# Kernel optimization log

Measured on AMD Instinct MI355X. Metric: run time of the kernel, lower is better.

Reference implementation:

```python
import jax, jax.numpy as jnp
import numpy as np

B, T, NC, NK, H, W = 2, 4, 3, 16, 180, 320
K = 3
PAD = 1
SCALE = 4
K2 = K * K
CIN_D = T * NK  # deformable conv input channels = group_of_frames * num_kernels


def conv2d(x, w, b=None, pad=PAD):
    y = jax.lax.conv_general_dilated(
        x, w, (1, 1), [(pad, pad), (pad, pad)],
        dimension_numbers=('NCHW', 'OIHW', 'NCHW'))
    if b is not None:
        y = y + b[None, :, None, None]
    return y


def convlstm(X, w, b, W_ci, W_cf, W_co):
    # X: (B, T, NC, H, W) -> (B, T, NK, H, W); peephole ConvLSTM
    Bn = X.shape[0]
    h0 = jnp.zeros((Bn, NK, H, W), X.dtype)
    c0 = jnp.zeros_like(h0)

    def step(carry, xt):
        h, c = carry
        g = conv2d(jnp.concatenate([xt, h], axis=1), w, b)  # (B, 4*NK, H, W)
        ig, fg, cg, og = jnp.split(g, 4, axis=1)
        i = jax.nn.sigmoid(ig + W_ci * c)
        f = jax.nn.sigmoid(fg + W_cf * c)
        c = f * c + i * jnp.tanh(cg)
        o = jax.nn.sigmoid(og + W_co * c)
        h = o * jnp.tanh(c)
        return (h, c), h

    _, hs = jax.lax.scan(step, (h0, c0), jnp.swapaxes(X, 0, 1))
    return jnp.swapaxes(hs, 0, 1)  # (B, T, NK, H, W)


def deform_conv(x, off_w, off_b, mod_w, mod_b, w, b):
    # Modulated deformable conv v2 (torchvision deform_conv2d semantics)
    Bn, Cin, Hi, Wi = x.shape
    off = conv2d(x, off_w, off_b).reshape(Bn, K2, 2, Hi, Wi)  # (dy, dx) per tap
    mask = 2.0 * jax.nn.sigmoid(conv2d(x, mod_w, mod_b))       # (B, K2, H, W)
    dy, dx = off[:, :, 0], off[:, :, 1]
    ky, kx = jnp.meshgrid(jnp.arange(K), jnp.arange(K), indexing='ij')
    base_y = jnp.arange(Hi, dtype=x.dtype)[None, None, :, None] - PAD + ky.reshape(1, K2, 1, 1).astype(x.dtype)
    base_x = jnp.arange(Wi, dtype=x.dtype)[None, None, None, :] - PAD + kx.reshape(1, K2, 1, 1).astype(x.dtype)
    py = base_y + dy  # (B, K2, H, W) float sampling positions
    px = base_x + dx
    y0 = jnp.floor(py)
    x0 = jnp.floor(px)

    def gather(yi, xi):
        valid = ((yi >= 0) & (yi < Hi) & (xi >= 0) & (xi < Wi)).astype(x.dtype)
        yc = jnp.clip(yi, 0, Hi - 1).astype(jnp.int32)
        xc = jnp.clip(xi, 0, Wi - 1).astype(jnp.int32)
        v = jax.vmap(lambda xb, yb, xib: xb[:, yb, xib])(x, yc, xc)  # (B, C, K2, H, W)
        return v * valid[:, None]

    wy1 = py - y0
    wx1 = px - x0
    samp = (((1 - wy1) * (1 - wx1))[:, None] * gather(y0, x0)
            + ((1 - wy1) * wx1)[:, None] * gather(y0, x0 + 1)
            + (wy1 * (1 - wx1))[:, None] * gather(y0 + 1, x0)
            + (wy1 * wx1)[:, None] * gather(y0 + 1, x0 + 1))
    samp = samp * mask[:, None]  # (B, Cin, K2, H, W)
    out = jnp.einsum('bckhw,ock->bohw', samp, w.reshape(w.shape[0], Cin, K2))
    return out + b[None, :, None, None]


def pixel_shuffle(x, r):
    Bn, Crr, Hi, Wi = x.shape
    C = Crr // (r * r)
    x = x.reshape(Bn, C, r, r, Hi, Wi).transpose(0, 1, 4, 2, 5, 3)
    return x.reshape(Bn, C, Hi * r, Wi * r)


def setup_inputs() -> dict:
    key = jax.random.key(0)
    ks = jax.random.split(key, 16)
    s = lambda k, shape, sc=0.05: jax.random.normal(k, shape, jnp.float32) * sc
    return {
        'X': jax.random.uniform(ks[0], (B, T, NC, H, W), jnp.float32),
        'lstm_w': s(ks[1], (4 * NK, NC + NK, K, K)),
        'lstm_b': s(ks[2], (4 * NK,)),
        'W_ci': s(ks[3], (NK, H, W)),
        'W_cf': s(ks[4], (NK, H, W)),
        'W_co': s(ks[5], (NK, H, W)),
        'off_w': s(ks[6], (2 * K2, CIN_D, K, K), 0.01),
        'off_b': jnp.zeros((2 * K2,), jnp.float32),
        'mod_w': s(ks[7], (K2, CIN_D, K, K), 0.01),
        'mod_b': jnp.zeros((K2,), jnp.float32),
        'def_w': s(ks[8], (NK, CIN_D, K, K)),
        'def_b': s(ks[9], (NK,)),
        'out_w': s(ks[10], (NC * SCALE ** 2, NK, K, K)),
        'out_b': s(ks[11], (NC * SCALE ** 2,)),
    }


def reference(X, lstm_w, lstm_b, W_ci, W_cf, W_co, off_w, off_b, mod_w, mod_b, def_w, def_b, out_w, out_b):
    hs = convlstm(X, lstm_w, lstm_b, W_ci, W_cf, W_co)   # (B, T, NK, H, W)
    x = hs.reshape(hs.shape[0], T * NK, H, W)            # chunk(dim=1)+squeeze+cat(dim=1)
    x = deform_conv(x, off_w, off_b, mod_w, mod_b, def_w, def_b)  # (B, NK, H, W)
    x = conv2d(x, out_w, out_b)                          # (B, NC*scale^2, H, W)
    return jnp.clip(pixel_shuffle(x, SCALE), 0.0, 255.0)
```

## Files before the change

kernel.cpp:

```cpp
#include <hip/hip_runtime.h>
#include <hip/hip_bf16.h>

#define Bn 2
#define Tn 4
#define NCc 3
#define NKc 16
#define Hc 180
#define Wc 320
#define HWc (Hc * Wc)
#define NPIX (Bn * HWc)
#define CIN_LSTM 19
#define GATES 64
#define CIN_D 64
#define TAPS_L (CIN_LSTM * 9)
#define TAPS_D (CIN_D * 9)
#define TAPS_O (NKc * 9)

typedef __hip_bfloat16 bf16;
typedef float f32x4 __attribute__((ext_vector_type(4)));
typedef float f32x2 __attribute__((ext_vector_type(2)));

__device__ __forceinline__ float getv(const float* p, long i) { return p[i]; }
__device__ __forceinline__ float getv(const bf16* p, long i) {
    unsigned int u = ((unsigned int)((const unsigned short*)p)[i]) << 16;
    return __uint_as_float(u);
}
__device__ __forceinline__ void putv(float* p, long i, float v) { p[i] = v; }
__device__ __forceinline__ void putv(bf16* p, long i, float v) { p[i] = __float2bfloat16(v); }
__device__ __forceinline__ float sigm(float x) { return 1.0f / (1.0f + __expf(-x)); }
__device__ __forceinline__ float tanh_(float x) { return 1.0f - 2.0f / (__expf(2.0f * x) + 1.0f); }

__device__ __forceinline__ void load4(const float* row, int x0, float* d) {
    const float4 v = *(const float4*)(row + x0);
    d[0] = v.x; d[1] = v.y; d[2] = v.z; d[3] = v.w;
}
__device__ __forceinline__ void load4(const bf16* row, int x0, float* d) {
    ushort4 u = *(const ushort4*)((const unsigned short*)row + x0);
    d[0] = __uint_as_float(((unsigned int)u.x) << 16);
    d[1] = __uint_as_float(((unsigned int)u.y) << 16);
    d[2] = __uint_as_float(((unsigned int)u.z) << 16);
    d[3] = __uint_as_float(((unsigned int)u.w) << 16);
}

__device__ __forceinline__ int xcd_chunked(int i, int nwg) {
    int q = nwg >> 3, r = nwg & 7;
    int xcd = i & 7, idx = i >> 3;
    return (xcd < r ? xcd * (q + 1) : r * (q + 1) + (xcd - r) * q) + idx;
}

__device__ __forceinline__ void om_wait()
{
    asm volatile("s_waitcnt vmcnt(0)" ::: "memory");
    __builtin_amdgcn_sched_barrier(0);
}

__device__ __forceinline__ void om6_issue(
    const float* a0p, const float* a1p, const float* a2p,
    const float* b0p, const float* b1p, const float* b2p,
    f32x4& A0, f32x4& A1, f32x4& A2, f32x4& B0, f32x4& B1, f32x4& B2)
{
    asm volatile(
        "global_load_dwordx4 %[A0], %[a0], off\n\t"
        "global_load_dwordx4 %[A1], %[a1], off\n\t"
        "global_load_dwordx4 %[A2], %[a2], off\n\t"
        "global_load_dwordx4 %[B0], %[b0], off\n\t"
        "global_load_dwordx4 %[B1], %[b1], off\n\t"
        "global_load_dwordx4 %[B2], %[b2], off\n\t"
        : [A0]"=&v"(A0), [A1]"=&v"(A1), [A2]"=&v"(A2),
          [B0]"=&v"(B0), [B1]"=&v"(B1), [B2]"=&v"(B2)
        : [a0]"v"(a0p), [a1]"v"(a1p), [a2]"v"(a2p),
          [b0]"v"(b0p), [b1]"v"(b1p), [b2]"v"(b2p));
}

__device__ __forceinline__ void lstm_issue12(
    const float* p0, const float* p1, const float* p2, const float* p3,
    f32x4& a0, float& l0, float& r0,
    f32x4& a1, float& l1, float& r1,
    f32x4& a2, float& l2, float& r2,
    f32x4& a3, float& l3, float& r3)
{
    asm volatile(
        "global_load_dwordx4 %[A0], %[P0], off\n\t"
        "global_load_dword   %[L0], %[P0], off offset:-4\n\t"
        "global_load_dword   %[R0], %[P0], off offset:16\n\t"
        "global_load_dwordx4 %[A1], %[P1], off\n\t"
        "global_load_dword   %[L1], %[P1], off offset:-4\n\t"
        "global_load_dword   %[R1], %[P1], off offset:16\n\t"
        "global_load_dwordx4 %[A2], %[P2], off\n\t"
        "global_load_dword   %[L2], %[P2], off offset:-4\n\t"
        "global_load_dword   %[R2], %[P2], off offset:16\n\t"
        "global_load_dwordx4 %[A3], %[P3], off\n\t"
        "global_load_dword   %[L3], %[P3], off offset:-4\n\t"
        "global_load_dword   %[R3], %[P3], off offset:16\n\t"
        : [A0]"=&v"(a0), [L0]"=&v"(l0), [R0]"=&v"(r0),
          [A1]"=&v"(a1), [L1]"=&v"(l1), [R1]"=&v"(r1),
          [A2]"=&v"(a2), [L2]"=&v"(l2), [R2]"=&v"(r2),
          [A3]"=&v"(a3), [L3]"=&v"(l3), [R3]"=&v"(r3)
        : [P0]"v"(p0), [P1]"v"(p1), [P2]"v"(p2), [P3]"v"(p3));
}

__device__ __forceinline__ void dfm_issue9w(
    const float* base, const int (&o)[9], f32x2 (&v)[9])
{
    asm volatile(
        "global_load_dwordx2 %[V0], %[O0], %[B]\n\t"
        "global_load_dwordx2 %[V1], %[O1], %[B]\n\t"
        "global_load_dwordx2 %[V2], %[O2], %[B]\n\t"
        "global_load_dwordx2 %[V3], %[O3], %[B]\n\t"
        "global_load_dwordx2 %[V4], %[O4], %[B]\n\t"
        "global_load_dwordx2 %[V5], %[O5], %[B]\n\t"
        "global_load_dwordx2 %[V6], %[O6], %[B]\n\t"
        "global_load_dwordx2 %[V7], %[O7], %[B]\n\t"
        "global_load_dwordx2 %[V8], %[O8], %[B]\n\t"
        : [V0]"=&v"(v[0]), [V1]"=&v"(v[1]), [V2]"=&v"(v[2]),
          [V3]"=&v"(v[3]), [V4]"=&v"(v[4]), [V5]"=&v"(v[5]),
          [V6]"=&v"(v[6]), [V7]"=&v"(v[7]), [V8]"=&v"(v[8])
        : [B]"s"(base),
          [O0]"v"(o[0]), [O1]"v"(o[1]), [O2]"v"(o[2]),
          [O3]"v"(o[3]), [O4]"v"(o[4]), [O5]"v"(o[5]),
          [O6]"v"(o[6]), [O7]"v"(o[7]), [O8]"v"(o[8]));
}

__global__ void __launch_bounds__(256) k_detect(const void* lstm_w_raw, int* flag)
{
    __shared__ int bad;
    if (threadIdx.x == 0) bad = 0;
    __syncthreads();
    const unsigned short* u = (const unsigned short*)lstm_w_raw;
    int local = 0;
    for (int i = threadIdx.x; i < GATES * TAPS_L; i += 256) {
        unsigned int f32 = ((unsigned int)u[i]) << 16;
        float v = __uint_as_float(f32);
        if (!(fabsf(v) <= 64.0f)) local = 1;
    }
    if (local) atomicOr(&bad, 1);
    __syncthreads();
    if (threadIdx.x == 0) flag[0] = bad ? 0 : 1;
}

template <typename S>
__device__ __forceinline__ void conv_plane2r(
    const S* __restrict__ src, int cin, int y0, int x0, int kc,
    const float* __restrict__ sw, float (&acc)[2][4][4])
{
    float xs[4][6];
#pragma unroll
    for (int r = 0; r < 4; r++) {
        int yy = y0 - 1 + r;
        if (yy >= 0 && yy < Hc) {
            const S* row = src + (long)yy * Wc;
            xs[r][0] = (x0 > 0) ? getv(row, x0 - 1) : 0.0f;
            load4(row, x0, &xs[r][1]);
            xs[r][5] = (x0 + 4 < Wc) ? getv(row, x0 + 4) : 0.0f;
        } else {
#pragma unroll
            for (int j = 0; j < 6; j++) xs[r][j] = 0.0f;
        }
    }
    float4 wq[9];
#pragma unroll
    for (int t9 = 0; t9 < 9; t9++)
        wq[t9] = *(const float4*)&sw[(((cin * 9 + t9) * 16) + kc) * 4];
#pragma unroll
    for (int ky = 0; ky < 3; ky++) {
#pragma unroll
        for (int kx = 0; kx < 3; kx++) {
            const float4 w = wq[ky * 3 + kx];
#pragma unroll
            for (int px = 0; px < 4; px++) {
                float v0 = xs[ky][px + kx];
                float v1 = xs[ky + 1][px + kx];
                acc[0][0][px] += w.x * v0;  acc[1][0][px] += w.x * v1;
                acc[0][1][px] += w.y * v0;  acc[1][1][px] += w.y * v1;
                acc[0][2][px] += w.z * v0;  acc[1][2][px] += w.z * v1;
                acc[0][3][px] += w.w * v0;  acc[1][3][px] += w.w * v1;
            }
        }
    }
}

template <typename T>
__device__ __forceinline__ void lstm2r_body(
    const T* __restrict__ X, const T* __restrict__ lstm_w, const T* __restrict__ lstm_b,
    const T* __restrict__ Wci, const T* __restrict__ Wcf, const T* __restrict__ Wco,
    float* __restrict__ c_buf, float* __restrict__ xcat, int t,
    float* sw, float* sb)
{
    for (int i = threadIdx.x; i < GATES * TAPS_L; i += 256) {
        int co = i / TAPS_L, tap = i - co * TAPS_L;
        int kc = co & 15, g = co >> 4;
        sw[(tap * 16 + kc) * 4 + g] = getv(lstm_w, i);
    }
    if (threadIdx.x < GATES) sb[threadIdx.x] = getv(lstm_b, threadIdx.x);
    __syncthreads();

    int blk = xcd_chunked(blockIdx.x, Bn * 90 * 5);
    int seg = blk % 5; int rem = blk / 5;
    int yp = rem % 90; int b = rem / 90;
    int y0 = yp * 2;
    int kc = threadIdx.x >> 4, pl = threadIdx.x & 15;
    int x0 = seg * 64 + pl * 4;

    float acc[2][4][4];
#pragma unroll
    for (int px = 0; px < 4; px++) {
#pragma unroll
        for (int r = 0; r < 2; r++) {
            acc[r][0][px] = sb[kc];
            acc[r][1][px] = sb[16 + kc];
            acc[r][2][px] = sb[32 + kc];
            acc[r][3][px] = sb[48 + kc];
        }
    }

    const T* xt = X + (long)(b * Tn + t) * NCc * HWc;
#pragma unroll 1
    for (int cin = 0; cin < NCc; cin++)
        conv_plane2r(xt + (long)cin * HWc, cin, y0, x0, kc, sw, acc);

    if (t > 0) {
        const float* hp = xcat + ((long)b * CIN_D + (t - 1) * NKc) * HWc;
        long ro[4]; float vm[4];
#pragma unroll
        for (int r = 0; r < 4; r++) {
            int yy = y0 - 1 + r;
            vm[r] = (yy >= 0 && yy < Hc) ? 1.0f : 0.0f;
            ro[r] = (long)min(max(yy, 0), Hc - 1) * Wc + x0;
        }
        const float m0 = (x0 > 0) ? 1.0f : 0.0f;
        const float m1 = (x0 + 4 < Wc) ? 1.0f : 0.0f;

#pragma unroll 1
        for (int cin = 0; cin < NKc; cin++) {
            const float* xc = hp + (long)cin * HWc;
            f32x4 a0, a1, a2, a3;
            float l0, l1, l2, l3, rh0, rh1, rh2, rh3;
            lstm_issue12(xc + ro[0], xc + ro[1], xc + ro[2], xc + ro[3],
                         a0, l0, rh0, a1, l1, rh1, a2, l2, rh2, a3, l3, rh3);
            float4 wq[9];
#pragma unroll
            for (int t9 = 0; t9 < 9; t9++)
                wq[t9] = *(const float4*)&sw[((((cin + NCc) * 9 + t9) * 16) + kc) * 4];
            om_wait();
            float xs[4][6];
#pragma unroll
            for (int r = 0; r < 4; r++) {
                const f32x4 a = (r == 0) ? a0 : (r == 1) ? a1 : (r == 2) ? a2 : a3;
                const float ll = (r == 0) ? l0 : (r == 1) ? l1 : (r == 2) ? l2 : l3;
                const float rr = (r == 0) ? rh0 : (r == 1) ? rh1 : (r == 2) ? rh2 : rh3;
                xs[r][0] = ll * vm[r] * m0;
                xs[r][1] = a.x * vm[r]; xs[r][2] = a.y * vm[r];
                xs[r][3] = a.z * vm[r]; xs[r][4] = a.w * vm[r];
                xs[r][5] = rr * vm[r] * m1;
            }
#pragma unroll
            for (int ky = 0; ky < 3; ky++) {
#pragma unroll
                for (int kx = 0; kx < 3; kx++) {
                    const float4 w = wq[ky * 3 + kx];
#pragma unroll
                    for (int px = 0; px < 4; px++) {
                        float v0 = xs[ky][px + kx];
                        float v1 = xs[ky + 1][px + kx];
                        acc[0][0][px] += w.x * v0;  acc[1][0][px] += w.x * v1;
                        acc[0][1][px] += w.y * v0;  acc[1][1][px] += w.y * v1;
                        acc[0][2][px] += w.z * v0;  acc[1][2][px] += w.z * v1;
                        acc[0][3][px] += w.w * v0;  acc[1][3][px] += w.w * v1;
                    }
                }
            }
        }
    }

#pragma unroll
    for (int r = 0; r < 2; r++) {
        int y = y0 + r;
        long pbase = (long)y * Wc + x0;
        float* cb = c_buf + (long)(b * NKc + kc) * HWc + pbase;
        float cprev[4];
        if (t > 0) {
            const float4 cv = *(const float4*)cb;
            cprev[0] = cv.x; cprev[1] = cv.y; cprev[2] = cv.z; cprev[3] = cv.w;
        } else {
            cprev[0] = cprev[1] = cprev[2] = cprev[3] = 0.0f;
        }
        float wci[4], wcf[4], wco[4];
        load4(Wci + (long)kc * HWc + pbase, 0, wci);
        load4(Wcf + (long)kc * HWc + pbase, 0, wcf);
        load4(Wco + (long)kc * HWc + pbase, 0, wco);

        float cn4[4], h4[4];
#pragma unroll
        for (int px = 0; px < 4; px++) {
            float ii = sigm(acc[r][0][px] + wci[px] * cprev[px]);
            float ff = sigm(acc[r][1][px] + wcf[px] * cprev[px]);
            float cn = ff * cprev[px] + ii * tanh_(acc[r][2][px]);
            float oo = sigm(acc[r][3][px] + wco[px] * cn);
            cn4[px] = cn; h4[px] = oo * tanh_(cn);
        }
        *(float4*)cb = make_float4(cn4[0], cn4[1], cn4[2], cn4[3]);
        *(float4*)(xcat + ((long)b * CIN_D + t * NKc + kc) * HWc + pbase) =
            make_float4(h4[0], h4[1], h4[2], h4[3]);
    }
}

__global__ void __launch_bounds__(256) k_lstm2(
    const void* X, const void* lstm_w, const void* lstm_b,
    const void* Wci, const void* Wcf, const void* Wco,
    const int* __restrict__ flag,
    float* c_buf, float* xcat, int t)
{
    __shared__ float sw[TAPS_L * GATES];
    __shared__ float sb[GATES];
    if (flag[0])
        lstm2r_body<bf16>((const bf16*)X, (const bf16*)lstm_w, (const bf16*)lstm_b,
                          (const bf16*)Wci, (const bf16*)Wcf, (const bf16*)Wco,
                          c_buf, xcat, t, sw, sb);
    else
        lstm2r_body<float>((const float*)X, (const float*)lstm_w, (const float*)lstm_b,
                           (const float*)Wci, (const float*)Wcf, (const float*)Wco,
                           c_buf, xcat, t, sw, sb);
}

template <typename T>
__device__ __forceinline__ void offmod18_body(
    const float* __restrict__ xcat,
    const T* __restrict__ off_w, const T* __restrict__ off_b,
    const T* __restrict__ mod_w, const T* __restrict__ mod_b,
    float* __restrict__ ob0, float* __restrict__ mb0,
    float* __restrict__ ob1, float* __restrict__ mb1,
    float* sw, float* sb, float* se)
{
    int rb = xcd_chunked(blockIdx.x, 900);
    int type = rb & 1;
    int half = (rb >> 1) & 1;
    int chunk = rb >> 2;
    const int nslot = type ? 12 : 16;

    const float *eLp[3], *eRp[3];
    {
        long pL = (long)chunk * 512;
        int b = (int)(pL / HWc); int pp = (int)(pL - (long)b * HWc);
        int y = pp / Wc, x = pp - (pp / Wc) * Wc;
#pragma unroll
        for (int ky = 0; ky < 3; ky++)
            eLp[ky] = xcat + ((long)b * CIN_D + half * 32) * HWc
                    + (long)min(max(y + ky - 1, 0), Hc - 1) * Wc + x - 1;
        long pR = (long)chunk * 512 + 511;
        b = (int)(pR / HWc); pp = (int)(pR - (long)b * HWc);
        y = pp / Wc; x = pp - (pp / Wc) * Wc;
#pragma unroll
        for (int ky = 0; ky < 3; ky++)
            eRp[ky] = xcat + ((long)b * CIN_D + half * 32) * HWc
                    + (long)min(max(y + ky - 1, 0), Hc - 1) * Wc + x + 1;
    }

    for (int i = threadIdx.x; i < 288 * nslot; i += 256) {
        int tl = i / nslot, j = i - tl * nslot;
        int o = type ? 16 + j : j;
        long gtap = (long)half * 288 + tl;
        float v = 0.0f;
        if (o < 18) v = getv(off_w, (long)o * TAPS_D + gtap);
        else if (o < 27) v = getv(mod_w, (long)(o - 18) * TAPS_D + gtap);
        sw[tl * nslot + j] = v;
    }
    for (int i = threadIdx.x; i < 192; i += 256) {
        int lc = i / 6, e = i - lc * 6;
        const float* bp = (e == 0) ? eLp[0] : (e == 1) ? eLp[1] : (e == 2) ? eLp[2]
                        : (e == 3) ? eRp[0] : (e == 4) ? eRp[1] : eRp[2];
        se[lc * 8 + e] = bp[(long)lc * HWc];
    }
    if (threadIdx.x < nslot) {
        int o = (type ? 16 : 0) + threadIdx.x;
        float bv = 0.0f;
        if (half == 0)
            bv = (o < 18) ? getv(off_b, o) : (o < 27 ? getv(mod_b, o - 18) : 0.0f);
        sb[threadIdx.x] = bv;
    }
    __syncthreads();

    int og = threadIdx.x >> 6, lane = threadIdx.x & 63;

    long pg[2]; pg[0] = (long)chunk * 512 + 4 * lane; pg[1] = pg[0] + 256;
    int bg[2], ppg[2];
    int yo[2][3]; float vm[2][3], mL[2], mR[2];
    const float* xbg[2];
#pragma unroll
    for (int g = 0; g < 2; g++) {
        int b = (int)(pg[g] / HWc);
        int pp = (int)(pg[g] - (long)b * HWc);
        int y = pp / Wc, x = pp - (pp / Wc) * Wc;
        bg[g] = b; ppg[g] = pp;
        xbg[g] = xcat + (long)b * CIN_D * HWc;
#pragma unroll
        for (int ky = 0; ky < 3; ky++) {
            int yy = y + ky - 1;
            vm[g][ky] = (yy >= 0 && yy < Hc) ? 1.0f : 0.0f;
            yo[g][ky] = min(max(yy, 0), Hc - 1) * Wc + x;
        }
        mL[g] = (x > 0) ? 1.0f : 0.0f;
        mR[g] = (x + 4 < Wc) ? 1.0f : 0.0f;
    }

    const int per = type ? 3 : 4;
    int jbase = og * per;
    const int upl = (lane + 63) & 63, dnl = (lane + 1) & 63;

    float acc[4][2][4];
#pragma unroll
    for (int j = 0; j < 4; j++) {
        float bv = (j < per) ? sb[jbase + j] : 0.0f;
#pragma unroll
        for (int g = 0; g < 2; g++)
#pragma unroll
            for (int px = 0; px < 4; px++) acc[j][g][px] = bv;
    }

    const long cbase = (long)half * 32 * HWc;
#pragma unroll 1
    for (int lc = 0; lc < 32; lc++) {
        const long coff = cbase + (long)lc * HWc;
        const float* c0 = xbg[0] + coff;
        const float* c1 = xbg[1] + coff;
        f32x4 A[3], B[3];
        om6_issue(c0 + yo[0][0], c0 + yo[0][1], c0 + yo[0][2],
                  c1 + yo[1][0], c1 + yo[1][1], c1 + yo[1][2],
                  A[0], A[1], A[2], B[0], B[1], B[2]);
        float el[3], er[3];
#pragma unroll
        for (int ky = 0; ky < 3; ky++) {
            el[ky] = se[lc * 8 + ky];
            er[ky] = se[lc * 8 + 3 + ky];
        }
        float4 wr4[9]; float3 wr3[9];
        if (type == 0) {
#pragma unroll
            for (int t9 = 0; t9 < 9; t9++)
                wr4[t9] = *(const float4*)&sw[(lc * 9 + t9) * 16 + jbase];
        } else {
#pragma unroll
            for (int t9 = 0; t9 < 9; t9++) {
                const float* wp = &sw[(lc * 9 + t9) * 12 + jbase];
                wr3[t9] = make_float3(wp[0], wp[1], wp[2]);
            }
        }
        om_wait();

        float xs0[3][6], xs1[3][6];
#pragma unroll
        for (int ky = 0; ky < 3; ky++) {
            float aw = A[ky].w, ax = A[ky].x, bw = B[ky].w, bx = B[ky].x;
            float sAw = __shfl(aw, upl);
            float sAx = __shfl(ax, dnl);
            float sBw = __shfl(bw, upl);
            float sBx = __shfl(bx, dnl);
            float B0x = __shfl(bx, 0);
            float A63w = __shfl(aw, 63);
            float g0l = (lane == 0) ? el[ky] : sAw;
            float g0r = (lane == 63) ? B0x : sAx;
            float g1l = (lane == 0) ? A63w : sBw;
            float g1r = (lane == 63) ? er[ky] : sBx;
            float v0 = vm[0][ky], v1 = vm[1][ky];
            xs0[ky][0] = g0l * v0 * mL[0];
            xs0[ky][1] = A[ky].x * v0; xs0[ky][2] = A[ky].y * v0;
            xs0[ky][3] = A[ky].z * v0; xs0[ky][4] = A[ky].w * v0;
            xs0[ky][5] = g0r * v0 * mR[0];
            xs1[ky][0] = g1l * v1 * mL[1];
            xs1[ky][1] = B[ky].x * v1; xs1[ky][2] = B[ky].y * v1;
            xs1[ky][3] = B[ky].z * v1; xs1[ky][4] = B[ky].w * v1;
            xs1[ky][5] = g1r * v1 * mR[1];
        }

        if (type == 0) {
#pragma unroll
            for (int ky = 0; ky < 3; ky++) {
#pragma unroll
                for (int kx = 0; kx < 3; kx++) {
                    const float4 wq = wr4[ky * 3 + kx];
#pragma unroll
                    for (int px = 0; px < 4; px++) {
                        float u = xs0[ky][px + kx];
                        acc[0][0][px] += wq.x * u;
                        acc[1][0][px] += wq.y * u;
                        acc[2][0][px] += wq.z * u;
                        acc[3][0][px] += wq.w * u;
                        float w2 = xs1[ky][px + kx];
                        acc[0][1][px] += wq.x * w2;
                        acc[1][1][px] += wq.y * w2;
                        acc[2][1][px] += wq.z * w2;
                        acc[3][1][px] += wq.w * w2;
                    }
                }
            }
        } else {
#pragma unroll
            for (int ky = 0; ky < 3; ky++) {
#pragma unroll
                for (int kx = 0; kx < 3; kx++) {
                    const float3 wq = wr3[ky * 3 + kx];
#pragma unroll
                    for (int px = 0; px < 4; px++) {
                        float u = xs0[ky][px + kx];
                        acc[0][0][px] += wq.x * u;
                        acc[1][0][px] += wq.y * u;
                        acc[2][0][px] += wq.z * u;
                        float w2 = xs1[ky][px + kx];
                        acc[0][1][px] += wq.x * w2;
                        acc[1][1][px] += wq.y * w2;
                        acc[2][1][px] += wq.z * w2;
                    }
                }
            }
        }
    }

    float* obuf = half ? ob1 : ob0;
    float* mbuf = half ? mb1 : mb0;
#pragma unroll
    for (int j = 0; j < 4; j++) {
        if (j >= per) break;
        int o = (type ? 16 : 0) + jbase + j;
        if (o >= 27) break;
        if (o < 18) {
#pragma unroll
            for (int g = 0; g < 2; g++) {
                float* dst = obuf + ((long)bg[g] * 18 + o) * HWc + ppg[g];
                *(float4*)dst = make_float4(acc[j][g][0], acc[j][g][1],
                                            acc[j][g][2], acc[j][g][3]);
            }
        } else {
#pragma unroll
            for (int g = 0; g < 2; g++) {
                float* dst = mbuf + ((long)bg[g] * 9 + (o - 18)) * HWc + ppg[g];
                *(float4*)dst = make_float4(acc[j][g][0], acc[j][g][1],
                                            acc[j][g][2], acc[j][g][3]);
            }
        }
    }
}

__global__ void __launch_bounds__(256) k_offmod(
    const float* xcat, const void* off_w, const void* off_b,
    const void* mod_w, const void* mod_b, const int* __restrict__ flag,
    float* ob0, float* mb0, float* ob1, float* mb1)
{
    __shared__ float sw[288 * 16];
    __shared__ float sb[16];
    __shared__ float se[32 * 8];
    if (flag[0])
        offmod18_body<bf16>(xcat, (const bf16*)off_w, (const bf16*)off_b,
                            (const bf16*)mod_w, (const bf16*)mod_b,
                            ob0, mb0, ob1, mb1, sw, sb, se);
    else
        offmod18_body<float>(xcat, (const float*)off_w, (const float*)off_b,
                             (const float*)mod_w, (const float*)mod_b,
                             ob0, mb0, ob1, mb1, sw, sb, se);
}

template <typename T>
__device__ __forceinline__ void deform6_body(
    const float* __restrict__ xcat,
    const float* __restrict__ ob0, const float* __restrict__ mb0,
    const float* __restrict__ ob1, const float* __restrict__ mb1,
    const T* __restrict__ def_w, const T* __restrict__ def_b,
    float* __restrict__ dcout, float* sw, float* sb)
{
    for (int i = threadIdx.x; i < NKc * TAPS_D; i += 256) {
        int co = i / TAPS_D;
        int tap = i - co * TAPS_D;
        sw[tap * NKc + co] = getv(def_w, i);
    }
    if (threadIdx.x < NKc) sb[threadIdx.x] = getv(def_b, threadIdx.x);
    __syncthreads();

    int blk = xcd_chunked(blockIdx.x, NPIX / 256);
    int idx0 = blk * 256;
    int b = idx0 / HWc;
    int p = idx0 - b * HWc + threadIdx.x;
    int y = p / Wc, x = p - (p / Wc) * Wc;

    float w00[9], w01[9], w10[9], w11[9];
    int o0[9], o1[9];
    float sel[9];
#pragma unroll
    for (int k = 0; k < 9; k++) {
        int ky = k / 3, kx = k - (k / 3) * 3;
        long oyi = ((long)b * 18 + 2 * k) * HWc + p;
        long oxi = ((long)b * 18 + 2 * k + 1) * HWc + p;
        long mi  = ((long)b * 9 + k) * HWc + p;
        float dy = ob0[oyi] + ob1[oyi];
        float dx = ob0[oxi] + ob1[oxi];
        float m = 2.0f * sigm(mb0[mi] + mb1[mi]);
        float py = (float)(y - 1 + ky) + dy;
        float px = (float)(x - 1 + kx) + dx;
        float y0f = floorf(py), x0f = floorf(px);
        int y0 = (int)y0f, x0 = (int)x0f;
        float wy1 = py - y0f, wx1 = px - x0f;
        float a00 = (1.0f - wy1) * (1.0f - wx1) * m;
        float a01 = (1.0f - wy1) * wx1 * m;
        float a10 = wy1 * (1.0f - wx1) * m;
        float a11 = wy1 * wx1 * m;
        bool vy0 = (y0 >= 0) && (y0 < Hc);
        bool vy1 = (y0 + 1 >= 0) && (y0 + 1 < Hc);
        bool vx0 = (x0 >= 0) && (x0 < Wc);
        bool vx1 = (x0 + 1 >= 0) && (x0 + 1 < Wc);
        w00[k] = (vy0 && vx0) ? a00 : 0.0f;
        w01[k] = (vy0 && vx1) ? a01 : 0.0f;
        w10[k] = (vy1 && vx0) ? a10 : 0.0f;
        w11[k] = (vy1 && vx1) ? a11 : 0.0f;
        int yc0 = min(max(y0, 0), Hc - 1);
        int yc1 = min(max(y0 + 1, 0), Hc - 1);
        int xc0 = min(max(x0, 0), Wc - 1);
        int xc1 = min(max(x0 + 1, 0), Wc - 1);
        o0[k] = (yc0 * Wc + xc0) * 4;
        o1[k] = (yc1 * Wc + xc0) * 4;
        sel[k] = (xc1 > xc0) ? 1.0f : 0.0f;
    }

    float acc[NKc];
#pragma unroll
    for (int i = 0; i < NKc; i++) acc[i] = sb[i];

    const float* xb = xcat + (long)b * CIN_D * HWc;
#pragma unroll 1
    for (int cin = 0; cin < CIN_D; cin++) {
        const float* xc = xb + (long)cin * HWc;
        f32x2 u0[9], u1[9];
        dfm_issue9w(xc, o0, u0);
        dfm_issue9w(xc, o1, u1);
        om_wait();
        float s[9];
#pragma unroll
        for (int k = 0; k < 9; k++) {
            float v01 = u0[k].x + sel[k] * (u0[k].y - u0[k].x);
            float v11 = u1[k].x + sel[k] * (u1[k].y - u1[k].x);
            s[k] = w00[k] * u0[k].x + w01[k] * v01 +
                   w10[k] * u1[k].x + w11[k] * v11;
        }
#pragma unroll
        for (int k = 0; k < 9; k++) {
            const float* wrow = &sw[(cin * 9 + k) * NKc];
#pragma unroll
            for (int co = 0; co < NKc; co++) acc[co] += wrow[co] * s[k];
        }
    }

#pragma unroll
    for (int co = 0; co < NKc; co++)
        dcout[((long)b * NKc + co) * HWc + p] = acc[co];
}

__global__ void __launch_bounds__(256) k_deform(
    const float* xcat, const float* ob0, const float* mb0,
    const float* ob1, const float* mb1,
    const void* def_w, const void* def_b, const int* __restrict__ flag,
    float* dcout)
{
    __shared__ float sw[TAPS_D * NKc];
    __shared__ float sb[NKc];
    if (flag[0])
        deform6_body<bf16>(xcat, ob0, mb0, ob1, mb1,
                           (const bf16*)def_w, (const bf16*)def_b, dcout, sw, sb);
    else
        deform6_body<float>(xcat, ob0, mb0, ob1, mb1,
                            (const float*)def_w, (const float*)def_b, dcout, sw, sb);
}

template <typename T>
__device__ __forceinline__ void outconv6_body(
    const float* __restrict__ dcout, const T* __restrict__ out_w,
    const T* __restrict__ out_b, T* __restrict__ out, float* sw, float* sb)
{
    int rb = xcd_chunked(blockIdx.x, 900);
    int type = rb & 1;
    int chunk = rb >> 1;

    for (int i = threadIdx.x; i < 24 * TAPS_O; i += 256) {
        int o = i / TAPS_O, tap = i - o * TAPS_O;
        int slot = (o / 6) * 8 + (o % 6);
        sw[tap * 32 + slot] = getv(out_w, (long)(type * 24 + o) * TAPS_O + tap);
    }
    if (threadIdx.x < 24) sb[threadIdx.x] = getv(out_b, type * 24 + threadIdx.x);
    __syncthreads();

    int og = threadIdx.x >> 6, lane = threadIdx.x & 63;
    long p0 = ((long)chunk * 64 + lane) * 4;
    int b = (int)(p0 / HWc);
    int p = (int)(p0 - (long)b * HWc);
    int y = p / Wc, x0 = p - (p / Wc) * Wc;

    float acc[6][4];
#pragma unroll
    for (int j = 0; j < 6; j++) {
        float bv = sb[og * 6 + j];
#pragma unroll
        for (int px = 0; px < 4; px++) acc[j][px] = bv;
    }

    const float* xb = dcout + (long)b * NKc * HWc;
#pragma unroll 1
    for (int cin = 0; cin < NKc; cin++) {
        const float* xc = xb + (long)cin * HWc;
        float xs[3][6];
#pragma unroll
        for (int ky = 0; ky < 3; ky++) {
            int yy = y + ky - 1;
            if (yy >= 0 && yy < Hc) {
                const float* row = xc + (long)yy * Wc;
                xs[ky][0] = (x0 > 0) ? row[x0 - 1] : 0.0f;
                load4(row, x0, &xs[ky][1]);
                xs[ky][5] = (x0 + 4 < Wc) ? row[x0 + 4] : 0.0f;
            } else {
#pragma unroll
                for (int j = 0; j < 6; j++) xs[ky][j] = 0.0f;
            }
        }
        float4 wa[9]; float2 wb[9];
#pragma unroll
        for (int t9 = 0; t9 < 9; t9++) {
            const float* wp = &sw[(cin * 9 + t9) * 32 + og * 8];
            wa[t9] = *(const float4*)wp;
            wb[t9] = *(const float2*)(wp + 4);
        }
#pragma unroll
        for (int ky = 0; ky < 3; ky++) {
#pragma unroll
            for (int kx = 0; kx < 3; kx++) {
                const float4 w0 = wa[ky * 3 + kx];
                const float2 w1 = wb[ky * 3 + kx];
#pragma unroll
                for (int px = 0; px < 4; px++) {
                    float v = xs[ky][px + kx];
                    acc[0][px] += w0.x * v;  acc[1][px] += w0.y * v;
                    acc[2][px] += w0.z * v;  acc[3][px] += w0.w * v;
                    acc[4][px] += w1.x * v;  acc[5][px] += w1.y * v;
                }
            }
        }
    }

#pragma unroll
    for (int j = 0; j < 6; j++) {
        int co = type * 24 + og * 6 + j;
        int cc = co >> 4;
        int r = co & 15;
        int ii = r >> 2, jj = r & 3;
        long ob = (((long)b * 3 + cc) * (Hc * 4) + (y * 4 + ii)) * (long)(Wc * 4);
#pragma unroll
        for (int px = 0; px < 4; px++) {
            float v = fminf(fmaxf(acc[j][px], 0.0f), 255.0f);
            putv(out, ob + (x0 + px) * 4 + jj, v);
        }
    }
}

__global__ void __launch_bounds__(256) k_outconv(
    const float* dcout, const void* out_w, const void* out_b,
    const int* __restrict__ flag, void* out)
{
    __shared__ float sw[TAPS_O * 32];
    __shared__ float sb[24];
    if (flag[0])
        outconv6_body<bf16>(dcout, (const bf16*)out_w, (const bf16*)out_b, (bf16*)out, sw, sb);
    else
        outconv6_body<float>(dcout, (const float*)out_w, (const float*)out_b, (float*)out, sw, sb);
}

extern "C" void kernel_launch(void* const* d_in, const int* in_sizes, int n_in,
                              void* d_out, int out_size, void* d_ws, size_t ws_size,
                              hipStream_t stream) {
    const void* X      = d_in[0];
    const void* lstm_w = d_in[1];
    const void* lstm_b = d_in[2];
    const void* Wci    = d_in[3];
    const void* Wcf    = d_in[4];
    const void* Wco    = d_in[5];
    const void* off_w  = d_in[6];
    const void* off_b  = d_in[7];
    const void* mod_w  = d_in[8];
    const void* mod_b  = d_in[9];
    const void* def_w  = d_in[10];
    const void* def_b  = d_in[11];
    const void* out_w  = d_in[12];
    const void* out_b  = d_in[13];

    int* flag = (int*)d_ws;
    float* W = (float*)d_ws + 64;
    size_t o = 0;
    float* c_buf   = W + o; o += (size_t)Bn * NKc * HWc;
    float* xcat    = W + o; o += (size_t)Bn * CIN_D * HWc;
    float* dcout   = W + o; o += (size_t)Bn * NKc * HWc;
    float* offbuf  = W + o; o += (size_t)Bn * 18 * HWc;
    float* maskbuf = W + o; o += (size_t)Bn * 9 * HWc;
    float* offbuf1  = W + o; o += (size_t)Bn * 18 * HWc;
    float* maskbuf1 = W + o; o += (size_t)Bn * 9 * HWc;

    dim3 blk(256);
    dim3 gridP(NPIX / 256);
    dim3 gridL2(Bn * (Hc / 2) * 5);
    dim3 gridOM(4 * (NPIX / 512));
    dim3 gridC2(2 * (NPIX / 4 / 64));

    k_detect<<<1, blk, 0, stream>>>(lstm_w, flag);
    for (int t = 0; t < Tn; t++) {
        k_lstm2<<<gridL2, blk, 0, stream>>>(X, lstm_w, lstm_b, Wci, Wcf, Wco,
                                            flag, c_buf, xcat, t);
    }
    k_offmod<<<gridOM, blk, 0, stream>>>(xcat, off_w, off_b, mod_w, mod_b, flag,
                                         offbuf, maskbuf, offbuf1, maskbuf1);
    k_deform<<<gridP, blk, 0, stream>>>(xcat, offbuf, maskbuf, offbuf1, maskbuf1,
                                        def_w, def_b, flag, dcout);
    k_outconv<<<gridC2, blk, 0, stream>>>(dcout, out_w, out_b, flag, d_out);
}
```

Baseline: 578.8 us.

## Stage offset/mask conv input rows into LDS with double-buffered async loads

```diff
diff --git a/kernel.cpp b/kernel.cpp
--- a/kernel.cpp
+++ b/kernel.cpp
@@ -54,22 +54,15 @@
     __builtin_amdgcn_sched_barrier(0);
 }
 
-__device__ __forceinline__ void om6_issue(
-    const float* a0p, const float* a1p, const float* a2p,
-    const float* b0p, const float* b1p, const float* b2p,
-    f32x4& A0, f32x4& A1, f32x4& A2, f32x4& B0, f32x4& B1, f32x4& B2)
-{
-    asm volatile(
-        "global_load_dwordx4 %[A0], %[a0], off\n\t"
-        "global_load_dwordx4 %[A1], %[a1], off\n\t"
-        "global_load_dwordx4 %[A2], %[a2], off\n\t"
-        "global_load_dwordx4 %[B0], %[b0], off\n\t"
-        "global_load_dwordx4 %[B1], %[b1], off\n\t"
-        "global_load_dwordx4 %[B2], %[b2], off\n\t"
-        : [A0]"=&v"(A0), [A1]"=&v"(A1), [A2]"=&v"(A2),
-          [B0]"=&v"(B0), [B1]"=&v"(B1), [B2]"=&v"(B2)
-        : [a0]"v"(a0p), [a1]"v"(a1p), [a2]"v"(a2p),
-          [b0]"v"(b0p), [b1]"v"(b1p), [b2]"v"(b2p));
+__device__ __forceinline__ void om_stage(const float* src, float* dst, int lane)
+{
+#pragma unroll
+    for (int k = 0; k < 4; k++) {
+        __builtin_amdgcn_global_load_lds(
+            (__attribute__((address_space(1))) const void*)(src + k * 256 + lane * 4),
+            (__attribute__((address_space(3))) void*)(dst + k * 256),
+            16, 0, 0);
+    }
 }
 
 __device__ __forceinline__ void lstm_issue12(
@@ -323,13 +316,13 @@
 }
 
 template <typename T>
-__device__ __forceinline__ void offmod18_body(
+__device__ __forceinline__ void offmod19_body(
     const float* __restrict__ xcat,
     const T* __restrict__ off_w, const T* __restrict__ off_b,
     const T* __restrict__ mod_w, const T* __restrict__ mod_b,
     float* __restrict__ ob0, float* __restrict__ mb0,
     float* __restrict__ ob1, float* __restrict__ mb1,
-    float* sw, float* sb, float* se)
+    float* sw, float* sb, float* se, float* sp)
 {
     int rb = xcd_chunked(blockIdx.x, 900);
     int type = rb & 1;
@@ -354,6 +347,19 @@
             eRp[ky] = xcat + ((long)b * CIN_D + half * 32) * HWc
                     + (long)min(max(y + ky - 1, 0), Hc - 1) * Wc + x + 1;
     }
+
+    const float* psrc[2];
+    int ppstart[2];
+#pragma unroll
+    for (int g = 0; g < 2; g++) {
+        long gs = (long)chunk * 512 + g * 256;
+        int bb = (int)(gs / HWc);
+        int pps = (int)(gs - (long)bb * HWc);
+        ppstart[g] = pps;
+        psrc[g] = xcat + ((long)bb * CIN_D + half * 32) * HWc + pps - 324;
+    }
+
+    int og = threadIdx.x >> 6, lane = threadIdx.x & 63;
 
     for (int i = threadIdx.x; i < 288 * nslot; i += 256) {
         int tl = i / nslot, j = i - tl * nslot;
@@ -377,26 +383,27 @@
             bv = (o < 18) ? getv(off_b, o) : (o < 27 ? getv(mod_b, o - 18) : 0.0f);
         sb[threadIdx.x] = bv;
     }
+    if (og == 0) {
+        om_stage(psrc[0], sp, lane);
+        om_stage(psrc[1], sp + 1024, lane);
+    }
     __syncthreads();
-
-    int og = threadIdx.x >> 6, lane = threadIdx.x & 63;
 
     long pg[2]; pg[0] = (long)chunk * 512 + 4 * lane; pg[1] = pg[0] + 256;
     int bg[2], ppg[2];
-    int yo[2][3]; float vm[2][3], mL[2], mR[2];
-    const float* xbg[2];
+    float vm[2][3], mL[2], mR[2];
+    int lo[2][3];
 #pragma unroll
     for (int g = 0; g < 2; g++) {
         int b = (int)(pg[g] / HWc);
         int pp = (int)(pg[g] - (long)b * HWc);
         int y = pp / Wc, x = pp - (pp / Wc) * Wc;
         bg[g] = b; ppg[g] = pp;
-        xbg[g] = xcat + (long)b * CIN_D * HWc;
 #pragma unroll
         for (int ky = 0; ky < 3; ky++) {
             int yy = y + ky - 1;
             vm[g][ky] = (yy >= 0 && yy < Hc) ? 1.0f : 0.0f;
-            yo[g][ky] = min(max(yy, 0), Hc - 1) * Wc + x;
+            lo[g][ky] = min(max(yy, 0), Hc - 1) * Wc + x - ppstart[g] + 324;
         }
         mL[g] = (x > 0) ? 1.0f : 0.0f;
         mR[g] = (x + 4 < Wc) ? 1.0f : 0.0f;
@@ -416,16 +423,21 @@
             for (int px = 0; px < 4; px++) acc[j][g][px] = bv;
     }
 
-    const long cbase = (long)half * 32 * HWc;
+    int cur = 0;
 #pragma unroll 1
     for (int lc = 0; lc < 32; lc++) {
-        const long coff = cbase + (long)lc * HWc;
-        const float* c0 = xbg[0] + coff;
-        const float* c1 = xbg[1] + coff;
+        const float* spc = sp + cur * 2048;
+        if (og == 0 && lc + 1 < 32) {
+            const long noff = (long)(lc + 1) * HWc;
+            om_stage(psrc[0] + noff, sp + (cur ^ 1) * 2048, lane);
+            om_stage(psrc[1] + noff, sp + (cur ^ 1) * 2048 + 1024, lane);
+        }
         f32x4 A[3], B[3];
-        om6_issue(c0 + yo[0][0], c0 + yo[0][1], c0 + yo[0][2],
-                  c1 + yo[1][0], c1 + yo[1][1], c1 + yo[1][2],
-                  A[0], A[1], A[2], B[0], B[1], B[2]);
+#pragma unroll
+        for (int ky = 0; ky < 3; ky++) {
+            A[ky] = *(const f32x4*)&spc[lo[0][ky]];
+            B[ky] = *(const f32x4*)&spc[1024 + lo[1][ky]];
+        }
         float el[3], er[3];
 #pragma unroll
         for (int ky = 0; ky < 3; ky++) {
@@ -444,7 +456,6 @@
                 wr3[t9] = make_float3(wp[0], wp[1], wp[2]);
             }
         }
-        om_wait();
 
         float xs0[3][6], xs1[3][6];
 #pragma unroll
@@ -512,6 +523,8 @@
                 }
             }
         }
+        __syncthreads();
+        cur ^= 1;
     }
 
     float* obuf = half ? ob1 : ob0;
@@ -547,14 +560,15 @@
     __shared__ float sw[288 * 16];
     __shared__ float sb[16];
     __shared__ float se[32 * 8];
+    __shared__ float sp[2 * 2048];
     if (flag[0])
-        offmod18_body<bf16>(xcat, (const bf16*)off_w, (const bf16*)off_b,
+        offmod19_body<bf16>(xcat, (const bf16*)off_w, (const bf16*)off_b,
                             (const bf16*)mod_w, (const bf16*)mod_b,
-                            ob0, mb0, ob1, mb1, sw, sb, se);
+                            ob0, mb0, ob1, mb1, sw, sb, se, sp);
     else
-        offmod18_body<float>(xcat, (const float*)off_w, (const float*)off_b,
+        offmod19_body<float>(xcat, (const float*)off_w, (const float*)off_b,
                              (const float*)mod_w, (const float*)mod_b,
-                             ob0, mb0, ob1, mb1, sw, sb, se);
+                             ob0, mb0, ob1, mb1, sw, sb, se, sp);
 }
 
 template <typename T>
```

Result: no change. 583.3 us (+0.8%).
